# Kernel tuning notes

Measured on AMD Instinct MI355X. Metric: run time of the kernel, lower is better.

## Reference

```python
import jax, jax.numpy as jnp
import numpy as np

B, V, L = 256, 128000, 2048
EPS = 1e-05


def setup_inputs() -> dict:
    key = jax.random.key(0)
    k1, k2, k3, k4, k5 = jax.random.split(key, 5)
    logits_next = jax.random.normal(k1, (B, V), jnp.float32)
    token_ids = jax.random.randint(k2, (B, L), 0, V, jnp.int32)
    presence_penalties = jax.random.uniform(k3, (B,), jnp.float32) * 1.5
    temperatures = jax.random.uniform(k4, (B,), jnp.float32, 0.5, 1.5)
    # make first quarter of the batch greedy (temperature == 0)
    temperatures = temperatures.at[: B // 4].set(0.0)
    u = jax.random.uniform(k5, (B, V), jnp.float32, 1e-9, 1.0)
    gumbel = -jnp.log(-jnp.log(u))  # Gumbel(0,1) noise for multinomial sampling
    return {
        "logits_next": logits_next,
        "token_ids": token_ids,
        "presence_penalties": presence_penalties,
        "temperatures": temperatures,
        "gumbel": gumbel,
    }


def reference(logits_next, token_ids, presence_penalties, temperatures, gumbel):
    Bn, Vn = logits_next.shape
    # presence mask: 1.0 where token id appeared in the history (counts > 0)
    rows = jnp.arange(Bn, dtype=jnp.int32)[:, None]  # [B,1]
    presence = jnp.zeros((Bn, Vn), logits_next.dtype).at[rows, token_ids].set(1.0)
    penalized = logits_next - presence_penalties[:, None] * presence

    greedy = temperatures < EPS  # [B]
    safe_t = jnp.where(greedy, jnp.float32(1.0), temperatures)
    scaled = penalized / safe_t[:, None]

    # greedy rows: plain argmax; sample rows: Gumbel-max == multinomial(softmax)
    greedy_tok = jnp.argmax(penalized, axis=-1)
    sampled_tok = jnp.argmax(scaled + gumbel, axis=-1)
    token_ids_next = jnp.where(greedy, greedy_tok, sampled_tok)
    return token_ids_next.astype(jnp.int32)
```

## Files before the change

### kernel.cpp

```cpp
#include <hip/hip_runtime.h>
#include <math.h>

#define BATCH 256
#define VOCAB 128000
#define HIST  2048
#define EPS_T 1e-5f

#define SEGS 5
#define SEG_ELEMS (VOCAB / SEGS)
#define SEG_VEC   (SEG_ELEMS / 4)
#define SEG_WORDS (SEG_ELEMS / 32)
#define BBLOCK 256
#define BWAVES (BBLOCK / 64)
#define NCHUNK (SEG_ELEMS / (BBLOCK * 4))
#define PF 4

typedef float f32x4 __attribute__((ext_vector_type(4)));

__device__ __forceinline__ void gload(f32x4& dst, const f32x4* addr) {
    asm volatile("global_load_dwordx4 %0, %1, off"
                 : "=&v"(dst) : "v"(addr) : "memory");
}

__device__ __forceinline__ unsigned fkey(float f) {
    unsigned b = __float_as_uint(f);
    return (b & 0x80000000u) ? ~b : (b | 0x80000000u);
}

__device__ __forceinline__ void upd(float s, int idx, float& best, int& besti) {
    if (s > best || (s == best && idx < besti)) { best = s; besti = idx; }
}

__device__ __forceinline__ void body4(f32x4 l, unsigned w, int sh, float pen,
                                      int idx0, float& best, int& besti) {
    #pragma unroll
    for (int j = 0; j < 4; j++) {
        float present = (float)((w >> (sh + j)) & 1u);
        float p = l[j] - pen * present;
        upd(p, idx0 + j, best, besti);
    }
}

__device__ __forceinline__ void body4s(f32x4 l, f32x4 g, unsigned w, int sh,
                                       float pen, float temp,
                                       int idx0, float& best, int& besti) {
    #pragma unroll
    for (int j = 0; j < 4; j++) {
        float present = (float)((w >> (sh + j)) & 1u);
        float p = l[j] - pen * present;
        float s = p / temp + g[j];
        upd(s, idx0 + j, best, besti);
    }
}

__device__ __forceinline__ void setbit(int t, int segBase, unsigned* smask) {
    unsigned u = (unsigned)(t - segBase);
    if (u < (unsigned)SEG_ELEMS)
        atomicOr(&smask[u >> 5], 1u << (u & 31));
}

__global__ __launch_bounds__(BBLOCK, 1) void fused_scan(
    const float* __restrict__ logits,
    const float* __restrict__ gumbel,
    const int*   __restrict__ token_ids,
    const float* __restrict__ penalties,
    const float* __restrict__ temps,
    unsigned long long* __restrict__ keys)
{
    __shared__ unsigned smask[SEG_WORDS];
    __shared__ float wval[BWAVES];
    __shared__ int   widx[BWAVES];

    const int blk = blockIdx.x;
    const int b   = blk / SEGS;
    const int seg = blk - b * SEGS;
    const int tid = threadIdx.x;

    const float pen    = penalties[b];
    const float temp   = temps[b];
    const bool  greedy = (temp < EPS_T);

    const int segBase = seg * SEG_ELEMS;

    const int4* rt = (const int4*)(token_ids + (size_t)b * HIST);
    int4 ta = rt[tid];
    int4 tb = rt[tid + BBLOCK];

    #pragma unroll
    for (int i = tid; i < SEG_WORDS; i += BBLOCK) smask[i] = 0u;
    __syncthreads();

    setbit(ta.x, segBase, smask); setbit(ta.y, segBase, smask);
    setbit(ta.z, segBase, smask); setbit(ta.w, segBase, smask);
    setbit(tb.x, segBase, smask); setbit(tb.y, segBase, smask);
    setbit(tb.z, segBase, smask); setbit(tb.w, segBase, smask);
    __syncthreads();

    const f32x4* lgp = (const f32x4*)(logits + (size_t)b * VOCAB) + seg * SEG_VEC + tid;
    const f32x4* gmp = (const f32x4*)(gumbel + (size_t)b * VOCAB) + seg * SEG_VEC + tid;

    float best  = -INFINITY;
    int   besti = 0x7fffffff;
    const int sh    = (tid * 4) & 31;
    const int abs0  = segBase + tid * 4;
    const int wbase = tid >> 3;

    if (greedy) {
        f32x4 lb[NCHUNK];
        #pragma unroll
        for (int k = 0; k < PF; ++k) gload(lb[k], lgp + k * BBLOCK);
        #pragma unroll
        for (int k = 0; k < NCHUNK; ++k) {
            if (k + PF < NCHUNK) gload(lb[k + PF], lgp + (k + PF) * BBLOCK);
            const int rem = (k + PF < NCHUNK) ? PF : (NCHUNK - 1 - k);
            asm volatile("s_waitcnt vmcnt(%0)" :: "i"(rem) : "memory");
            __builtin_amdgcn_sched_barrier(0);
            unsigned w = smask[wbase + 32 * k];
            body4(lb[k], w, sh, pen, abs0 + k * BBLOCK * 4, best, besti);
        }
    } else {
        f32x4 lb[NCHUNK], gb[NCHUNK];
        #pragma unroll
        for (int k = 0; k < PF; ++k) {
            gload(lb[k], lgp + k * BBLOCK);
            gload(gb[k], gmp + k * BBLOCK);
        }
        #pragma unroll
        for (int k = 0; k < NCHUNK; ++k) {
            if (k + PF < NCHUNK) {
                gload(lb[k + PF], lgp + (k + PF) * BBLOCK);
                gload(gb[k + PF], gmp + (k + PF) * BBLOCK);
            }
            const int rem = (k + PF < NCHUNK) ? PF : (NCHUNK - 1 - k);
            asm volatile("s_waitcnt vmcnt(%0)" :: "i"(2 * rem) : "memory");
            __builtin_amdgcn_sched_barrier(0);
            unsigned w = smask[wbase + 32 * k];
            body4s(lb[k], gb[k], w, sh, pen, temp,
                   abs0 + k * BBLOCK * 4, best, besti);
        }
    }

    #pragma unroll
    for (int off = 32; off > 0; off >>= 1) {
        float ov = __shfl_down(best, off, 64);
        int   oi = __shfl_down(besti, off, 64);
        if (ov > best || (ov == best && oi < besti)) { best = ov; besti = oi; }
    }
    const int wave = tid >> 6, lane = tid & 63;
    if (lane == 0) { wval[wave] = best; widx[wave] = besti; }
    __syncthreads();

    if (tid == 0) {
        #pragma unroll
        for (int wv = 1; wv < BWAVES; wv++) {
            if (wval[wv] > best || (wval[wv] == best && widx[wv] < besti)) {
                best = wval[wv]; besti = widx[wv];
            }
        }
        unsigned long long key =
            ((unsigned long long)fkey(best) << 32) | (unsigned)(~besti);
        atomicMax(keys + b, key);
    }
}

__global__ void decode_kernel(const unsigned long long* __restrict__ keys,
                              int* __restrict__ out)
{
    const int b = threadIdx.x;
    out[b] = (int)(~(unsigned)keys[b]);
}

extern "C" void kernel_launch(void* const* d_in, const int* in_sizes, int n_in,
                              void* d_out, int out_size, void* d_ws, size_t ws_size,
                              hipStream_t stream) {
    const float* logits    = (const float*)d_in[0];
    const int*   token_ids = (const int*)d_in[1];
    const float* penalties = (const float*)d_in[2];
    const float* temps     = (const float*)d_in[3];
    const float* gumbel    = (const float*)d_in[4];
    int* out = (int*)d_out;

    unsigned long long* keys = (unsigned long long*)d_ws;

    hipMemsetAsync(keys, 0, BATCH * sizeof(unsigned long long), stream);

    fused_scan<<<BATCH * SEGS, BBLOCK, 0, stream>>>(logits, gumbel, token_ids,
                                                    penalties, temps, keys);
    decode_kernel<<<1, BATCH, 0, stream>>>(keys, out);
}
```

Measured before the change: 275.7 us.

## Interleave vocab chunks across waves with full-row presence mask per block

Work is now split as 8 blocks per row instead of 5 contiguous segments, and each of the 32 waves per row strides over 256-element chunks with a simple one-ahead software prefetch using nontemporal loads instead of the fully unrolled inline-asm prefetch with explicit waitcnt. Each block builds the presence bitmask for the whole vocab in shared memory (16 KB), which drops the segment range check. The block-level shared-memory reduction is replaced by one atomicMax per wave. In exchange each block repeats the full-row mask build, more atomics hit global memory, and there is less memory-level parallelism per thread.

```diff
diff --git a/kernel.cpp b/kernel.cpp
--- a/kernel.cpp
+++ b/kernel.cpp
@@ -6,21 +6,14 @@
 #define HIST  2048
 #define EPS_T 1e-5f
 
-#define SEGS 5
-#define SEG_ELEMS (VOCAB / SEGS)
-#define SEG_VEC   (SEG_ELEMS / 4)
-#define SEG_WORDS (SEG_ELEMS / 32)
 #define BBLOCK 256
-#define BWAVES (BBLOCK / 64)
-#define NCHUNK (SEG_ELEMS / (BBLOCK * 4))
-#define PF 4
+#define BLOCKS_PER_ROW 8
+#define GRID (BATCH * BLOCKS_PER_ROW)
+#define WAVES_PER_ROW (BLOCKS_PER_ROW * 4)
+#define CHUNKS (VOCAB / 256)
+#define MASK_WORDS (VOCAB / 32)
 
 typedef float f32x4 __attribute__((ext_vector_type(4)));
-
-__device__ __forceinline__ void gload(f32x4& dst, const f32x4* addr) {
-    asm volatile("global_load_dwordx4 %0, %1, off"
-                 : "=&v"(dst) : "v"(addr) : "memory");
-}
 
 __device__ __forceinline__ unsigned fkey(float f) {
     unsigned b = __float_as_uint(f);
@@ -53,12 +46,6 @@
     }
 }
 
-__device__ __forceinline__ void setbit(int t, int segBase, unsigned* smask) {
-    unsigned u = (unsigned)(t - segBase);
-    if (u < (unsigned)SEG_ELEMS)
-        atomicOr(&smask[u >> 5], 1u << (u & 31));
-}
-
 __global__ __launch_bounds__(BBLOCK, 1) void fused_scan(
     const float* __restrict__ logits,
     const float* __restrict__ gumbel,
@@ -67,76 +54,71 @@
     const float* __restrict__ temps,
     unsigned long long* __restrict__ keys)
 {
-    __shared__ unsigned smask[SEG_WORDS];
-    __shared__ float wval[BWAVES];
-    __shared__ int   widx[BWAVES];
+    __shared__ unsigned smask[MASK_WORDS];
 
-    const int blk = blockIdx.x;
-    const int b   = blk / SEGS;
-    const int seg = blk - b * SEGS;
-    const int tid = threadIdx.x;
+    const int blk  = blockIdx.x;
+    const int row  = blk >> 3;
+    const int tid  = threadIdx.x;
+    const int lane = tid & 63;
+    const int wave = tid >> 6;
+    const int wir  = ((blk & 7) << 2) | wave;
 
-    const float pen    = penalties[b];
-    const float temp   = temps[b];
+    const float pen    = penalties[row];
+    const float temp   = temps[row];
     const bool  greedy = (temp < EPS_T);
 
-    const int segBase = seg * SEG_ELEMS;
-
-    const int4* rt = (const int4*)(token_ids + (size_t)b * HIST);
+    const int4* rt = (const int4*)(token_ids + (size_t)row * HIST);
     int4 ta = rt[tid];
     int4 tb = rt[tid + BBLOCK];
 
-    #pragma unroll
-    for (int i = tid; i < SEG_WORDS; i += BBLOCK) smask[i] = 0u;
+    for (int i = tid; i < MASK_WORDS; i += BBLOCK) smask[i] = 0u;
     __syncthreads();
 
-    setbit(ta.x, segBase, smask); setbit(ta.y, segBase, smask);
-    setbit(ta.z, segBase, smask); setbit(ta.w, segBase, smask);
-    setbit(tb.x, segBase, smask); setbit(tb.y, segBase, smask);
-    setbit(tb.z, segBase, smask); setbit(tb.w, segBase, smask);
+    atomicOr(&smask[ta.x >> 5], 1u << (ta.x & 31));
+    atomicOr(&smask[ta.y >> 5], 1u << (ta.y & 31));
+    atomicOr(&smask[ta.z >> 5], 1u << (ta.z & 31));
+    atomicOr(&smask[ta.w >> 5], 1u << (ta.w & 31));
+    atomicOr(&smask[tb.x >> 5], 1u << (tb.x & 31));
+    atomicOr(&smask[tb.y >> 5], 1u << (tb.y & 31));
+    atomicOr(&smask[tb.z >> 5], 1u << (tb.z & 31));
+    atomicOr(&smask[tb.w >> 5], 1u << (tb.w & 31));
     __syncthreads();
 
-    const f32x4* lgp = (const f32x4*)(logits + (size_t)b * VOCAB) + seg * SEG_VEC + tid;
-    const f32x4* gmp = (const f32x4*)(gumbel + (size_t)b * VOCAB) + seg * SEG_VEC + tid;
+    const f32x4* Lr = (const f32x4*)(logits + (size_t)row * VOCAB);
+    const f32x4* Gr = (const f32x4*)(gumbel + (size_t)row * VOCAB);
 
     float best  = -INFINITY;
     int   besti = 0x7fffffff;
-    const int sh    = (tid * 4) & 31;
-    const int abs0  = segBase + tid * 4;
-    const int wbase = tid >> 3;
+    const int sh    = (lane & 7) * 4;
+    const int wsub  = lane >> 3;
 
     if (greedy) {
-        f32x4 lb[NCHUNK];
-        #pragma unroll
-        for (int k = 0; k < PF; ++k) gload(lb[k], lgp + k * BBLOCK);
-        #pragma unroll
-        for (int k = 0; k < NCHUNK; ++k) {
-            if (k + PF < NCHUNK) gload(lb[k + PF], lgp + (k + PF) * BBLOCK);
-            const int rem = (k + PF < NCHUNK) ? PF : (NCHUNK - 1 - k);
-            asm volatile("s_waitcnt vmcnt(%0)" :: "i"(rem) : "memory");
-            __builtin_amdgcn_sched_barrier(0);
-            unsigned w = smask[wbase + 32 * k];
-            body4(lb[k], w, sh, pen, abs0 + k * BBLOCK * 4, best, besti);
+        int c = wir;
+        f32x4 lc = __builtin_nontemporal_load(Lr + c * 64 + lane);
+        while (true) {
+            const int cn = c + 32;
+            f32x4 ln = lc;
+            if (cn < CHUNKS) ln = __builtin_nontemporal_load(Lr + cn * 64 + lane);
+            const unsigned w = smask[c * 8 + wsub];
+            body4(lc, w, sh, pen, c * 256 + lane * 4, best, besti);
+            if (cn >= CHUNKS) break;
+            lc = ln; c = cn;
         }
     } else {
-        f32x4 lb[NCHUNK], gb[NCHUNK];
-        #pragma unroll
-        for (int k = 0; k < PF; ++k) {
-            gload(lb[k], lgp + k * BBLOCK);
-            gload(gb[k], gmp + k * BBLOCK);
-        }
-        #pragma unroll
-        for (int k = 0; k < NCHUNK; ++k) {
-            if (k + PF < NCHUNK) {
-                gload(lb[k + PF], lgp + (k + PF) * BBLOCK);
-                gload(gb[k + PF], gmp + (k + PF) * BBLOCK);
+        int c = wir;
+        f32x4 lc = __builtin_nontemporal_load(Lr + c * 64 + lane);
+        f32x4 gc = __builtin_nontemporal_load(Gr + c * 64 + lane);
+        while (true) {
+            const int cn = c + 32;
+            f32x4 ln = lc, gn = gc;
+            if (cn < CHUNKS) {
+                ln = __builtin_nontemporal_load(Lr + cn * 64 + lane);
+                gn = __builtin_nontemporal_load(Gr + cn * 64 + lane);
             }
-            const int rem = (k + PF < NCHUNK) ? PF : (NCHUNK - 1 - k);
-            asm volatile("s_waitcnt vmcnt(%0)" :: "i"(2 * rem) : "memory");
-            __builtin_amdgcn_sched_barrier(0);
-            unsigned w = smask[wbase + 32 * k];
-            body4s(lb[k], gb[k], w, sh, pen, temp,
-                   abs0 + k * BBLOCK * 4, best, besti);
+            const unsigned w = smask[c * 8 + wsub];
+            body4s(lc, gc, w, sh, pen, temp, c * 256 + lane * 4, best, besti);
+            if (cn >= CHUNKS) break;
+            lc = ln; gc = gn; c = cn;
         }
     }
 
@@ -146,20 +128,11 @@
         int   oi = __shfl_down(besti, off, 64);
         if (ov > best || (ov == best && oi < besti)) { best = ov; besti = oi; }
     }
-    const int wave = tid >> 6, lane = tid & 63;
-    if (lane == 0) { wval[wave] = best; widx[wave] = besti; }
-    __syncthreads();
 
-    if (tid == 0) {
-        #pragma unroll
-        for (int wv = 1; wv < BWAVES; wv++) {
-            if (wval[wv] > best || (wval[wv] == best && widx[wv] < besti)) {
-                best = wval[wv]; besti = widx[wv];
-            }
-        }
+    if (lane == 0) {
         unsigned long long key =
             ((unsigned long long)fkey(best) << 32) | (unsigned)(~besti);
-        atomicMax(keys + b, key);
+        atomicMax(keys + row, key);
     }
 }
 
@@ -184,7 +157,7 @@
 
     hipMemsetAsync(keys, 0, BATCH * sizeof(unsigned long long), stream);
 
-    fused_scan<<<BATCH * SEGS, BBLOCK, 0, stream>>>(logits, gumbel, token_ids,
-                                                    penalties, temps, keys);
+    fused_scan<<<GRID, BBLOCK, 0, stream>>>(logits, gumbel, token_ids,
+                                            penalties, temps, keys);
     decode_kernel<<<1, BATCH, 0, stream>>>(keys, out);
 }
```

Measured after the change: 252.4 us. -8.4%, faster.
